# Optimization experiments

Measured on AMD Instinct MI355X. Metric: run time of the kernel, lower is better.

The kernel has to match this reference:

```python
import jax, jax.numpy as jnp
import numpy as np

H, W = 512, 512
FEAT_LEVELS = [3, 4, 5, 6, 7]
NEG_THRESH, POS_THRESH = 0.4, 0.5
N_GT = 1024


def make_priors():
    """Prior boxes in cxcywh, same order as the torch itertools.product loops."""
    out = []
    for lvl in FEAT_LEVELS:
        s = 2 ** lvl
        ys = np.arange(s // 2, H, s, dtype=np.float32)
        xs = np.arange(s // 2, W, s, dtype=np.float32)
        cy, cx = np.meshgrid(ys, xs, indexing='ij')          # row-major over (cy, cx)
        centers = np.stack([cx.ravel(), cy.ravel()], axis=-1)  # [C, 2] = (cx, cy)
        wh = []
        for aspect in [0.5, 1.0, 2.0]:
            for scale in [0.0, 1.0 / 3.0, 2.0 / 3.0]:
                h = 4 * s * (2.0 ** scale) * np.sqrt(aspect)
                w = 4 * s * (2.0 ** scale) / np.sqrt(aspect)
                wh.append([w, h])
        wh = np.asarray(wh, np.float32)                       # [9, 2]
        C = centers.shape[0]
        cxy = np.repeat(centers, 9, axis=0)                   # [C*9, 2]
        whr = np.tile(wh, (C, 1))                             # [C*9, 2]
        out.append(np.concatenate([cxy, whr], axis=-1))
    return np.concatenate(out, axis=0).astype(np.float32)     # [M, 4]


def cxcywh_to_xyxy(b):
    cx, cy, w, h = b[..., 0], b[..., 1], b[..., 2], b[..., 3]
    return jnp.stack([cx - w / 2, cy - h / 2, cx + w / 2, cy + h / 2], axis=-1)


def xyxy_to_cxcywh(b):
    x1, y1, x2, y2 = b[..., 0], b[..., 1], b[..., 2], b[..., 3]
    return jnp.stack([(x1 + x2) / 2, (y1 + y2) / 2, x2 - x1, y2 - y1], axis=-1)


def box_iou(a, b):
    # a: [N,4], b: [M,4] (xyxy) -> [N,M]
    area_a = (a[:, 2] - a[:, 0]) * (a[:, 3] - a[:, 1])
    area_b = (b[:, 2] - b[:, 0]) * (b[:, 3] - b[:, 1])
    lt = jnp.maximum(a[:, None, :2], b[None, :, :2])   # [N,M,2]
    rb = jnp.minimum(a[:, None, 2:], b[None, :, 2:])
    wh = jnp.clip(rb - lt, 0.0)
    inter = wh[..., 0] * wh[..., 1]
    return inter / (area_a[:, None] + area_b[None, :] - inter)


def setup_inputs() -> dict:
    key = jax.random.key(0)
    k1, k2, k3, k4 = jax.random.split(key, 4)
    cx = jax.random.uniform(k1, (N_GT,), jnp.float32, 16.0, float(W) - 16.0)
    cy = jax.random.uniform(k2, (N_GT,), jnp.float32, 16.0, float(H) - 16.0)
    wh = jax.random.uniform(k3, (N_GT, 2), jnp.float32, 8.0, 256.0)
    bboxes = jnp.stack([cx - wh[:, 0] / 2, cy - wh[:, 1] / 2,
                        cx + wh[:, 0] / 2, cy + wh[:, 1] / 2], axis=-1)
    labels = jax.random.randint(k4, (N_GT,), 1, 81, dtype=jnp.int64 if jax.config.jax_enable_x64 else jnp.int32)
    priors = jnp.asarray(make_priors())
    return {"bboxes": bboxes, "labels": labels, "priors": priors}


def reference(bboxes, labels, priors):
    n = bboxes.shape[0]
    ious = box_iou(bboxes, cxcywh_to_xyxy(priors))          # [N, M]
    max_ious = ious.max(axis=0)                             # [M]
    match_ids = ious.argmax(axis=0)                         # [M]
    force_assign_ids = ious.argmax(axis=1)                  # [N]
    match_ids = match_ids.at[force_assign_ids].set(jnp.arange(n))
    max_ious = max_ious.at[force_assign_ids].set(POS_THRESH)

    matched = xyxy_to_cxcywh(bboxes)[match_ids]             # [M, 4]
    dcx = (matched[..., 0] - priors[..., 0]) / priors[..., 2] / 0.1
    dcy = (matched[..., 1] - priors[..., 1]) / priors[..., 3] / 0.1
    dw = jnp.log(matched[..., 2] / priors[..., 2]) / 0.2
    dh = jnp.log(matched[..., 3] / priors[..., 3]) / 0.2
    reg_targets = jnp.stack([dcx, dcy, dw, dh], axis=-1)    # [M, 4]

    cls_targets = labels[match_ids]
    cls_targets = jnp.where(max_ious < POS_THRESH, -1, cls_targets)
    cls_targets = jnp.where(max_ious < NEG_THRESH, 0, cls_targets)
    return reg_targets, cls_targets
```

## Files before the change

kernel.cpp:

```cpp
#include <hip/hip_runtime.h>


static constexpr float NEG_THRESH = 0.4f;
static constexpr float POS_THRESH = 0.5f;
static constexpr int N_GT = 1024;
static constexpr int GT_PER_BLK = 64;
static constexpr int NCHUNK = N_GT / GT_PER_BLK;
static constexpr int MPAD = 49152;
static constexpr int BLK = 256;
static constexpr int NB = MPAD / BLK;
static constexpr int T_ROWS = 16;
static constexpr int STRIDE = 264;

__device__ __forceinline__ unsigned long long packiou(float iou, unsigned idx_) {
    return ((unsigned long long)__float_as_uint(iou) << 32) |
           (unsigned long long)(0xFFFFFFFFu - idx_);
}

__global__ void __launch_bounds__(256) init_kernel(
        unsigned long long* __restrict__ part1,
        unsigned long long* __restrict__ partG,
        int* __restrict__ force_n) {
    int i = blockIdx.x * 256 + threadIdx.x;
    part1[i] = 0x00000000FFFFFFFFull;
    force_n[i] = -1;
    if (i < N_GT) partG[i] = 0ull;
}

__global__ void __launch_bounds__(256) fused_kernel(
        const float* __restrict__ bboxes,
        const float* __restrict__ priors,
        unsigned long long* __restrict__ part1,
        unsigned long long* __restrict__ partG,
        int M) {
#pragma clang fp contract(off)
    __shared__ float tile[T_ROWS][STRIDE];
    __shared__ float4 sgbox[GT_PER_BLK];
    __shared__ float2 sgmeta[GT_PER_BLK];
    __shared__ float sbb[4][4];
    __shared__ int scount;

    int tid = threadIdx.x;
    int lane = tid & 63;
    int wid = tid >> 6;
    int bx = (NB - 1) - blockIdx.y;
    int n0 = blockIdx.x * GT_PER_BLK;
    int m = bx * BLK + tid;
    bool valid = (m < M);

    float4 p = valid ? reinterpret_cast<const float4*>(priors)[m]
                     : make_float4(0.f, 0.f, 0.f, 0.f);
    float bx1 = p.x - p.z / 2.0f;
    float by1 = p.y - p.w / 2.0f;
    float bx2 = p.x + p.z / 2.0f;
    float by2 = p.y + p.w / 2.0f;
    float area_b = (bx2 - bx1) * (by2 - by1);

    float mnx = valid ? bx1 : 1e30f;
    float mny = valid ? by1 : 1e30f;
    float mxx = valid ? bx2 : -1e30f;
    float mxy = valid ? by2 : -1e30f;
#pragma unroll
    for (int mk = 1; mk < 64; mk <<= 1) {
        mnx = fminf(mnx, __shfl_xor(mnx, mk));
        mny = fminf(mny, __shfl_xor(mny, mk));
        mxx = fmaxf(mxx, __shfl_xor(mxx, mk));
        mxy = fmaxf(mxy, __shfl_xor(mxy, mk));
    }
    if (lane == 0) {
        sbb[wid][0] = mnx; sbb[wid][1] = mny; sbb[wid][2] = mxx; sbb[wid][3] = mxy;
    }
    __syncthreads();

    if (tid < 64) {
        float BX1 = fminf(fminf(sbb[0][0], sbb[1][0]), fminf(sbb[2][0], sbb[3][0]));
        float BY1 = fminf(fminf(sbb[0][1], sbb[1][1]), fminf(sbb[2][1], sbb[3][1]));
        float BX2 = fmaxf(fmaxf(sbb[0][2], sbb[1][2]), fmaxf(sbb[2][2], sbb[3][2]));
        float BY2 = fmaxf(fmaxf(sbb[0][3], sbb[1][3]), fmaxf(sbb[2][3], sbb[3][3]));
        float4 g = reinterpret_cast<const float4*>(bboxes)[n0 + tid];
        bool hit = (g.x < BX2) & (g.z > BX1) & (g.y < BY2) & (g.w > BY1);
        unsigned long long bal = __ballot(hit);
        if (hit) {
            int pos = __popcll(bal & ((1ull << tid) - 1ull));
            sgbox[pos] = g;
            sgmeta[pos] = make_float2((g.z - g.x) * (g.w - g.y), (float)tid);
        }
        if (tid == 0) scount = __popcll(bal);
    }
    __syncthreads();
    int cnt = scount;

    float4 gl = sgbox[lane & 63];
    bool hw = (lane < cnt) & (gl.x < mxx) & (gl.z > mnx) &
              (gl.y < mxy) & (gl.w > mny);
    unsigned long long wavemask = __ballot(hw);

    float best = 0.0f;
    int bestn = n0;

    int row = tid >> 4;
    int sub = tid & 15;
    int m0 = bx * BLK;

    int nfull = cnt >> 4;
    int tail = cnt & 15;

    for (int b = 0; b <= nfull; ++b) {
        int rows = (b < nfull) ? T_ROWS : tail;
        if (rows == 0) break;
        int base = b * T_ROWS;

#pragma unroll
        for (int r = 0; r < T_ROWS; ++r) {
            if (r < rows) {
                int idx = base + r;
                if ((wavemask >> idx) & 1) {
                    float4 gb = sgbox[idx];
                    float2 mt = sgmeta[idx];
                    int jn = n0 + (int)mt.y;

                    float ltx = fmaxf(gb.x, bx1);
                    float lty = fmaxf(gb.y, by1);
                    float rbx = fminf(gb.z, bx2);
                    float rby = fminf(gb.w, by2);
                    float w = rbx - ltx; if (w < 0.0f) w = 0.0f;
                    float h = rby - lty; if (h < 0.0f) h = 0.0f;
                    float inter = w * h;
                    float iou = inter / (mt.x + area_b - inter);

                    if (iou > best) { best = iou; bestn = jn; }
                    tile[r][tid] = valid ? iou : -1.0f;
                } else {
                    tile[r][tid] = -1.0f;
                }
            } else {
                tile[r][tid] = -1.0f;
            }
        }
        __syncthreads();

        float bi = -2.0f;
        int bm = 0;
#pragma unroll
        for (int k = 0; k < BLK / 16; ++k) {
            int col = sub + 16 * k;
            float v = tile[row][col];
            if (v > bi) { bi = v; bm = col; }
        }
#pragma unroll
        for (int msk = 1; msk < 16; msk <<= 1) {
            float oi = __shfl_xor(bi, msk);
            int om = __shfl_xor(bm, msk);
            if (oi > bi || (oi == bi && om < bm)) { bi = oi; bm = om; }
        }
        if (sub == 0 && bi > 0.0f) {
            int jr = (int)sgmeta[base + row].y;
            atomicMax(&partG[n0 + jr], packiou(bi, (unsigned)(m0 + bm)));
        }
        __syncthreads();
    }

    if (valid && best > 0.0f) {
        atomicMax(&part1[m], packiou(best, (unsigned)bestn));
    }
}

__global__ void rs_kernel(const unsigned long long* __restrict__ partG,
                          int* __restrict__ force_n) {
    int n = blockIdx.x * blockDim.x + threadIdx.x;
    if (n >= N_GT) return;
    unsigned long long v = partG[n];
    int m = (int)(0xFFFFFFFFu - (unsigned)(v & 0xFFFFFFFFull));
    atomicMax(&force_n[m], n);
}

__global__ void __launch_bounds__(256) encode_kernel(
        const float* __restrict__ bboxes,
        const int* __restrict__ labels,
        const float* __restrict__ priors,
        const unsigned long long* __restrict__ part1,
        const int* __restrict__ force_n,
        float* __restrict__ out, int M) {
#pragma clang fp contract(off)
    int m = blockIdx.x * 256 + threadIdx.x;
    if (m >= M) return;

    unsigned long long v = part1[m];
    float iou = __uint_as_float((unsigned)(v >> 32));
    int mid = (int)(0xFFFFFFFFu - (unsigned)(v & 0xFFFFFFFFull));

    int f = force_n[m];
    if (f >= 0) { mid = f; iou = POS_THRESH; }

    float4 g = reinterpret_cast<const float4*>(bboxes)[mid];
    float mcx = (g.x + g.z) / 2.0f;
    float mcy = (g.y + g.w) / 2.0f;
    float mw = g.z - g.x;
    float mh = g.w - g.y;

    float4 p = reinterpret_cast<const float4*>(priors)[m];
    float dcx = ((mcx - p.x) / p.z) / 0.1f;
    float dcy = ((mcy - p.y) / p.w) / 0.1f;
    float dw = logf(mw / p.z) / 0.2f;
    float dh = logf(mh / p.w) / 0.2f;

    reinterpret_cast<float4*>(out)[m] = make_float4(dcx, dcy, dw, dh);

    int cls = labels[mid];
    if (iou < POS_THRESH) cls = -1;
    if (iou < NEG_THRESH) cls = 0;
    out[(size_t)4 * M + m] = (float)cls;
}

extern "C" void kernel_launch(void* const* d_in, const int* in_sizes, int n_in,
                              void* d_out, int out_size, void* d_ws, size_t ws_size,
                              hipStream_t stream) {
    const float* bboxes = (const float*)d_in[0];
    const int* labels = (const int*)d_in[1];
    const float* priors = (const float*)d_in[2];
    int M = in_sizes[2] / 4;
    float* out = (float*)d_out;

    char* ws = (char*)d_ws;
    unsigned long long* part1 = (unsigned long long*)ws;
    unsigned long long* partG = (unsigned long long*)(ws + (size_t)MPAD * 8);
    int* force_n = (int*)(ws + (size_t)MPAD * 8 + (size_t)N_GT * 8);

    init_kernel<<<MPAD / 256, 256, 0, stream>>>(part1, partG, force_n);
    fused_kernel<<<dim3(NCHUNK, NB), 256, 0, stream>>>(bboxes, priors, part1,
                                                       partG, M);
    rs_kernel<<<(N_GT + 255) / 256, 256, 0, stream>>>(partG, force_n);
    encode_kernel<<<(MPAD + 255) / 256, 256, 0, stream>>>(bboxes, labels, priors,
                                                          part1, force_n, out, M);
}
```

Measured before the change: 34.58 us.

## Replace global atomics with per-chunk partial buffers and drop init kernel

Each block now writes its per-prior best and per-GT best into dedicated partial slots instead of using global atomicMax, and the force_n reset moves into the fused kernel, so the separate init launch goes away. The rs kernel reduces 192 partial GT slots per box, and the encode kernel reduces 16 partial prior slots per prior. This removes one launch and the atomic contention. In exchange it adds workspace traffic: about 6 MB of partials written and reread, plus a serial 192-step loop per thread in rs_kernel.

```diff
diff --git a/kernel.cpp b/kernel.cpp
--- a/kernel.cpp
+++ b/kernel.cpp
@@ -17,34 +17,27 @@
            (unsigned long long)(0xFFFFFFFFu - idx_);
 }
 
-__global__ void __launch_bounds__(256) init_kernel(
-        unsigned long long* __restrict__ part1,
-        unsigned long long* __restrict__ partG,
-        int* __restrict__ force_n) {
-    int i = blockIdx.x * 256 + threadIdx.x;
-    part1[i] = 0x00000000FFFFFFFFull;
-    force_n[i] = -1;
-    if (i < N_GT) partG[i] = 0ull;
-}
-
 __global__ void __launch_bounds__(256) fused_kernel(
         const float* __restrict__ bboxes,
         const float* __restrict__ priors,
-        unsigned long long* __restrict__ part1,
-        unsigned long long* __restrict__ partG,
+        unsigned long long* __restrict__ part1c,
+        unsigned long long* __restrict__ partGc,
+        int* __restrict__ force_n,
         int M) {
 #pragma clang fp contract(off)
     __shared__ float tile[T_ROWS][STRIDE];
     __shared__ float4 sgbox[GT_PER_BLK];
     __shared__ float2 sgmeta[GT_PER_BLK];
+    __shared__ unsigned long long swin[GT_PER_BLK];
     __shared__ float sbb[4][4];
     __shared__ int scount;
 
     int tid = threadIdx.x;
     int lane = tid & 63;
     int wid = tid >> 6;
+    int cx = blockIdx.x;
     int bx = (NB - 1) - blockIdx.y;
-    int n0 = blockIdx.x * GT_PER_BLK;
+    int n0 = cx * GT_PER_BLK;
     int m = bx * BLK + tid;
     bool valid = (m < M);
 
@@ -86,6 +79,7 @@
             sgmeta[pos] = make_float2((g.z - g.x) * (g.w - g.y), (float)tid);
         }
         if (tid == 0) scount = __popcll(bal);
+        swin[tid] = 0ull;
     }
     __syncthreads();
     int cnt = scount;
@@ -155,22 +149,32 @@
         }
         if (sub == 0 && bi > 0.0f) {
             int jr = (int)sgmeta[base + row].y;
-            atomicMax(&partG[n0 + jr], packiou(bi, (unsigned)(m0 + bm)));
+            swin[jr] = packiou(bi, (unsigned)(m0 + bm));
         }
         __syncthreads();
     }
 
-    if (valid && best > 0.0f) {
-        atomicMax(&part1[m], packiou(best, (unsigned)bestn));
-    }
-}
-
-__global__ void rs_kernel(const unsigned long long* __restrict__ partG,
+    if (tid < GT_PER_BLK) {
+        partGc[(size_t)bx * N_GT + n0 + tid] = swin[tid];
+    }
+    if (valid) {
+        part1c[(size_t)cx * MPAD + m] = packiou(best, (unsigned)bestn);
+    }
+    if (cx == 0) {
+        force_n[bx * BLK + tid] = -1;
+    }
+}
+
+__global__ void rs_kernel(const unsigned long long* __restrict__ partGc,
                           int* __restrict__ force_n) {
     int n = blockIdx.x * blockDim.x + threadIdx.x;
     if (n >= N_GT) return;
-    unsigned long long v = partG[n];
-    int m = (int)(0xFFFFFFFFu - (unsigned)(v & 0xFFFFFFFFull));
+    unsigned long long best = 0ull;
+    for (int c = 0; c < NB; ++c) {
+        unsigned long long v = partGc[(size_t)c * N_GT + n];
+        if (v > best) best = v;
+    }
+    int m = (int)(0xFFFFFFFFu - (unsigned)(best & 0xFFFFFFFFull));
     atomicMax(&force_n[m], n);
 }
 
@@ -178,16 +182,20 @@
         const float* __restrict__ bboxes,
         const int* __restrict__ labels,
         const float* __restrict__ priors,
-        const unsigned long long* __restrict__ part1,
+        const unsigned long long* __restrict__ part1c,
         const int* __restrict__ force_n,
         float* __restrict__ out, int M) {
 #pragma clang fp contract(off)
     int m = blockIdx.x * 256 + threadIdx.x;
     if (m >= M) return;
 
-    unsigned long long v = part1[m];
-    float iou = __uint_as_float((unsigned)(v >> 32));
-    int mid = (int)(0xFFFFFFFFu - (unsigned)(v & 0xFFFFFFFFull));
+    unsigned long long best = part1c[m];
+    for (int c = 1; c < NCHUNK; ++c) {
+        unsigned long long v = part1c[(size_t)c * MPAD + m];
+        if (v > best) best = v;
+    }
+    float iou = __uint_as_float((unsigned)(best >> 32));
+    int mid = (int)(0xFFFFFFFFu - (unsigned)(best & 0xFFFFFFFFull));
 
     int f = force_n[m];
     if (f >= 0) { mid = f; iou = POS_THRESH; }
@@ -222,14 +230,15 @@
     float* out = (float*)d_out;
 
     char* ws = (char*)d_ws;
-    unsigned long long* part1 = (unsigned long long*)ws;
-    unsigned long long* partG = (unsigned long long*)(ws + (size_t)MPAD * 8);
-    int* force_n = (int*)(ws + (size_t)MPAD * 8 + (size_t)N_GT * 8);
-
-    init_kernel<<<MPAD / 256, 256, 0, stream>>>(part1, partG, force_n);
-    fused_kernel<<<dim3(NCHUNK, NB), 256, 0, stream>>>(bboxes, priors, part1,
-                                                       partG, M);
-    rs_kernel<<<(N_GT + 255) / 256, 256, 0, stream>>>(partG, force_n);
+    unsigned long long* part1c = (unsigned long long*)ws;
+    unsigned long long* partGc =
+        (unsigned long long*)(ws + (size_t)NCHUNK * MPAD * 8);
+    int* force_n =
+        (int*)(ws + (size_t)NCHUNK * MPAD * 8 + (size_t)NB * N_GT * 8);
+
+    fused_kernel<<<dim3(NCHUNK, NB), 256, 0, stream>>>(bboxes, priors, part1c,
+                                                       partGc, force_n, M);
+    rs_kernel<<<(N_GT + 255) / 256, 256, 0, stream>>>(partGc, force_n);
     encode_kernel<<<(MPAD + 255) / 256, 256, 0, stream>>>(bboxes, labels, priors,
-                                                          part1, force_n, out, M);
-}
+                                                          part1c, force_n, out, M);
+}
```

Result: slower. 42.27 us (+22.3%).
